# Performance work log

Measured on AMD Instinct MI355X. Metric: run time of the kernel, lower is better.

Reference implementation:

```python
import jax, jax.numpy as jnp
import numpy as np


def setup_inputs() -> dict:
    key = jax.random.key(0)
    ks = jax.random.split(key, 8)
    B, E, R, D, H = 8, 50000, 1000, 128, 256
    return {
        "head": jax.random.randint(ks[0], (B,), 0, E),
        "relation": jax.random.randint(ks[1], (B,), 0, R),
        "k": 10,
        "ent_emb": jax.random.normal(ks[2], (E, D), jnp.float32),
        "rel_emb": jax.random.normal(ks[3], (R, D), jnp.float32),
        "W1": jax.random.normal(ks[4], (3 * D, H), jnp.float32) * 0.05,
        "b1": jax.random.normal(ks[5], (H,), jnp.float32) * 0.05,
        "W2": jax.random.normal(ks[6], (H,), jnp.float32) * 0.05,
        "b2": jax.random.normal(ks[7], (1,), jnp.float32) * 0.05,
    }


def reference(head, relation, k, ent_emb, rel_emb, W1, b1, W2, b2):
    D = ent_emb.shape[1]
    # score_net first layer on cat([h, r, t]) == h@W1h + r@W1r + t@W1t (same math,
    # avoids materializing the [B*E, 3D] concat).
    W1h, W1r, W1t = W1[:D], W1[D:2 * D], W1[2 * D:]
    h = ent_emb[head]            # [B, D]
    r = rel_emb[relation]        # [B, D]
    ph = h @ W1h + r @ W1r + b1  # [B, H] -- head/relation part, computed once
    pt = ent_emb @ W1t           # [E, H] -- tail part over all entities
    hidden = jax.nn.relu(ph[:, None, :] + pt[None, :, :])   # [B, E, H]
    scores = jnp.einsum('beh,h->be', hidden, W2) + b2[0]     # [B, E]
    top_scores, top_indices = jax.lax.top_k(scores, k)
    return top_indices, top_scores
```

## Files before the change

### kernel.cpp

```cpp
#include <hip/hip_runtime.h>

#define D 128
#define HDIM 256
#define NB 8
#define NSHARD 32
#define CPS 16
#define NCAND (NSHARD * CPS)
#define PHW 16
#define WPAD 136

typedef short bf16x8 __attribute__((ext_vector_type(8)));
typedef float f32x4 __attribute__((ext_vector_type(4)));

__device__ __forceinline__ unsigned short f2bf(float x) {
    unsigned u = __float_as_uint(x);
    unsigned r = u + 0x7FFF + ((u >> 16) & 1);
    return (unsigned short)(r >> 16);
}
__device__ __forceinline__ bf16x8 pack_bf8(float4 u, float4 v) {
    union { bf16x8 v8; unsigned short s[8]; } r;
    r.s[0] = f2bf(u.x); r.s[1] = f2bf(u.y); r.s[2] = f2bf(u.z); r.s[3] = f2bf(u.w);
    r.s[4] = f2bf(v.x); r.s[5] = f2bf(v.y); r.s[6] = f2bf(v.z); r.s[7] = f2bf(v.w);
    return r.v8;
}

__device__ __forceinline__ unsigned long long sk_encode(float v, int idx) {
    unsigned u = __float_as_uint(v);
    u = (u & 0x80000000u) ? ~u : (u | 0x80000000u);
    return ((unsigned long long)u << 32) | (unsigned)(0xFFFFFFFFu - (unsigned)idx);
}
__device__ __forceinline__ float sk_val(unsigned long long key) {
    const unsigned u = (unsigned)(key >> 32);
    return (u & 0x80000000u) ? __uint_as_float(u & 0x7FFFFFFFu) : __uint_as_float(~u);
}
__device__ __forceinline__ int sk_idx(unsigned long long key) {
    return (int)(0xFFFFFFFFu - (unsigned)(key & 0xFFFFFFFFu));
}
__device__ __forceinline__ unsigned long long wave_max64(unsigned long long m) {
#pragma unroll
    for (int s = 32; s > 0; s >>= 1) {
        const unsigned long long o = __shfl_xor(m, s, 64);
        if (o > m) m = o;
    }
    return m;
}

__global__ __launch_bounds__(HDIM) void prep_kernel(
        const int* __restrict__ head, const int* __restrict__ relation,
        const float* __restrict__ ent_emb, const float* __restrict__ rel_emb,
        const float* __restrict__ W1, const float* __restrict__ b1,
        const float* __restrict__ W2, float* __restrict__ phW,
        unsigned short* __restrict__ w1tt) {
    const int w = blockIdx.x;
    const int tid = threadIdx.x;
    if (w < NB) {
        const int b = w;
        const long hidx = head[b];
        const long ridx = relation[b];
        const float* hrow = ent_emb + hidx * D;
        const float* rrow = rel_emb + ridx * D;
        float acc = b1[tid];
#pragma unroll 8
        for (int d = 0; d < D; ++d)
            acc += hrow[d] * W1[d * HDIM + tid];
#pragma unroll 8
        for (int d = 0; d < D; ++d)
            acc += rrow[d] * W1[(D + d) * HDIM + tid];
        phW[tid * PHW + b] = acc;
        if (b == 0) phW[tid * PHW + 8] = W2[tid];
    } else {
        const int k0 = (w - NB) * 4;
        const float* w1t = W1 + 2 * D * HDIM;
        unsigned short pk[4];
#pragma unroll
        for (int j = 0; j < 4; ++j)
            pk[j] = f2bf(w1t[(k0 + j) * HDIM + tid]);
        *(ushort4*)(w1tt + tid * D + k0) = make_ushort4(pk[0], pk[1], pk[2], pk[3]);
    }
}

__global__ __launch_bounds__(512, 2) void score_kernel(
        const float* __restrict__ ent_emb, const unsigned short* __restrict__ w1tt,
        const float* __restrict__ phW, float* __restrict__ scores, int E) {
    __shared__ __align__(16) unsigned short wL[HDIM][WPAD];
    __shared__ float phB[NB][HDIM];
    __shared__ float w2L[HDIM];

    const int tid = threadIdx.x;
    const int lane = tid & 63;
    const int wave = tid >> 6;
    const int lm = lane & 15;
    const int q = lane >> 4;
    const int base_e = blockIdx.x * 128 + wave * 16;

    const float* arow = ent_emb + (size_t)min(base_e + lm, E - 1) * D;
    bf16x8 aF[4];
#pragma unroll
    for (int kk = 0; kk < 4; ++kk) {
        const float4 u = *(const float4*)(arow + kk * 32 + q * 8);
        const float4 v = *(const float4*)(arow + kk * 32 + q * 8 + 4);
        aF[kk] = pack_bf8(u, v);
    }

#pragma unroll
    for (int i = 0; i < 8; ++i) {
        const int c = i * 512 + tid;
        const int row = c >> 4;
        const int col = (c & 15) << 3;
        *(uint4*)(&wL[row][col]) = *(const uint4*)(w1tt + row * D + col);
    }
    if (tid < HDIM) {
        const float4 p0 = *(const float4*)(phW + tid * PHW);
        const float4 p1 = *(const float4*)(phW + tid * PHW + 4);
        phB[0][tid] = p0.x; phB[1][tid] = p0.y; phB[2][tid] = p0.z; phB[3][tid] = p0.w;
        phB[4][tid] = p1.x; phB[5][tid] = p1.y; phB[6][tid] = p1.z; phB[7][tid] = p1.w;
        w2L[tid] = phW[tid * PHW + 8];
    }
    __syncthreads();

    float sp[NB * 4];
#pragma unroll
    for (int i = 0; i < NB * 4; ++i) sp[i] = 0.f;

#pragma unroll
    for (int t = 0; t < 16; ++t) {
        const int h = t * 16 + lm;
        bf16x8 bF[4];
#pragma unroll
        for (int kk = 0; kk < 4; ++kk)
            bF[kk] = *(const bf16x8*)(&wL[h][kk * 32 + q * 8]);

        float phv[8];
#pragma unroll
        for (int b = 0; b < NB; ++b) phv[b] = phB[b][h];
        const float w2v = w2L[h];

        f32x4 acc = (f32x4){0.f, 0.f, 0.f, 0.f};
#pragma unroll
        for (int kk = 0; kk < 4; ++kk)
            acc = __builtin_amdgcn_mfma_f32_16x16x32_bf16(aF[kk], bF[kk], acc, 0, 0, 0);

#pragma unroll
        for (int b = 0; b < NB; ++b)
#pragma unroll
            for (int r = 0; r < 4; ++r)
                sp[b * 4 + r] += fmaxf(phv[b] + acc[r], 0.f) * w2v;
    }

#pragma unroll
    for (int m = 1; m <= 8; m <<= 1) {
#pragma unroll
        for (int i = 0; i < NB * 4; ++i)
            sp[i] += __shfl_xor(sp[i], m, 64);
    }
    if (lm == 0) {
#pragma unroll
        for (int r = 0; r < 4; ++r) {
            const int e = base_e + q * 4 + r;
            if (e < E) {
#pragma unroll
                for (int b = 0; b < NB; ++b)
                    scores[(size_t)b * E + e] = sp[b * 4 + r];
            }
        }
    }
}

__global__ __launch_bounds__(256) void topk_rescore_kernel(
        const float* __restrict__ scores, int E,
        const float* __restrict__ ent_emb, const float* __restrict__ W1,
        const float* __restrict__ phW, const float* __restrict__ b2,
        unsigned long long* __restrict__ cand_exact) {
    const int b = blockIdx.x >> 5;
    const int s = blockIdx.x & 31;
    const int tid = threadIdx.x;
    const int lane = tid & 63;
    const int wave = tid >> 6;

    __shared__ unsigned long long cl[4 * CPS];
    __shared__ unsigned long long candk[CPS];
    __shared__ int eIdxs[CPS];
    __shared__ float entR[CPS][D];
    __shared__ float red[4][CPS];

    {
        const int shard = (E + NSHARD - 1) / NSHARD;
        const int start = s * shard;
        const int end = min(E, start + shard);
        const float* row = scores + (size_t)b * E;

        unsigned long long keys[CPS];
#pragma unroll
        for (int i = 0; i < CPS; ++i) keys[i] = 0ull;

        for (int e = start + tid; e < end; e += 256) {
            unsigned long long key = sk_encode(row[e], e);
            if (key > keys[CPS - 1]) {
#pragma unroll
                for (int j = 0; j < CPS; ++j) {
                    const bool gt = key > keys[j];
                    const unsigned long long mx = gt ? key : keys[j];
                    key = gt ? keys[j] : key;
                    keys[j] = mx;
                }
            }
        }
        for (int r = 0; r < CPS; ++r) {
            const unsigned long long m = wave_max64(keys[0]);
            if (keys[0] == m) {
#pragma unroll
                for (int j = 0; j < CPS - 1; ++j) keys[j] = keys[j + 1];
                keys[CPS - 1] = 0ull;
            }
            if (lane == 0) cl[wave * CPS + r] = m;
        }
        __syncthreads();
        if (wave == 0) {
            unsigned long long v = cl[lane];
            for (int r = 0; r < CPS; ++r) {
                const unsigned long long m = wave_max64(v);
                if (v == m) v = 0ull;
                if (lane == 0) candk[r] = m;
            }
        }
        __syncthreads();
    }

    if (tid < CPS) eIdxs[tid] = sk_idx(candk[tid]);
    __syncthreads();
    for (int t = tid; t < CPS * (D / 4); t += 256) {
        const int row = t >> 5, c4 = (t & 31) * 4;
        *(float4*)(&entR[row][c4]) =
            *(const float4*)(ent_emb + (size_t)eIdxs[row] * D + c4);
    }
    __syncthreads();

    const float* w1t = W1 + 2 * D * HDIM;
    float acc[CPS];
#pragma unroll
    for (int c = 0; c < CPS; ++c) acc[c] = 0.f;
    for (int d0 = 0; d0 < D; d0 += 4) {
        float w[4];
#pragma unroll
        for (int j = 0; j < 4; ++j) w[j] = w1t[(d0 + j) * HDIM + tid];
#pragma unroll
        for (int c = 0; c < CPS; ++c) {
            const float4 f = *(const float4*)(&entR[c][d0]);
            acc[c] += f.x * w[0] + f.y * w[1] + f.z * w[2] + f.w * w[3];
        }
    }
    const float phv = phW[tid * PHW + b];
    const float w2v = phW[tid * PHW + 8];
    float sc[CPS];
#pragma unroll
    for (int c = 0; c < CPS; ++c) sc[c] = fmaxf(acc[c] + phv, 0.f) * w2v;

#pragma unroll
    for (int m = 1; m <= 32; m <<= 1)
#pragma unroll
        for (int c = 0; c < CPS; ++c) sc[c] += __shfl_xor(sc[c], m, 64);
    if (lane == 0)
#pragma unroll
        for (int c = 0; c < CPS; ++c) red[wave][c] = sc[c];
    __syncthreads();
    if (tid < CPS) {
        const float v = red[0][tid] + red[1][tid] + red[2][tid] + red[3][tid] + b2[0];
        cand_exact[(size_t)(b * NSHARD + s) * CPS + tid] = sk_encode(v, eIdxs[tid]);
    }
}

__global__ __launch_bounds__(256) void final_kernel(
        const unsigned long long* __restrict__ cand_exact, int k,
        float* __restrict__ out) {
    const int lane = threadIdx.x & 63;
    const int wave = threadIdx.x >> 6;
    for (int b = wave; b < NB; b += 4) {
        unsigned long long lk[8];
#pragma unroll
        for (int j = 0; j < 8; ++j)
            lk[j] = cand_exact[(size_t)b * NCAND + j * 64 + lane];
#pragma unroll
        for (int i = 0; i < 8; ++i)
#pragma unroll
            for (int j = 0; j < 7; ++j)
                if (lk[j] < lk[j + 1]) {
                    const unsigned long long t = lk[j];
                    lk[j] = lk[j + 1];
                    lk[j + 1] = t;
                }
        for (int r = 0; r < k; ++r) {
            const unsigned long long m = wave_max64(lk[0]);
            if (lk[0] == m) {
#pragma unroll
                for (int j = 0; j < 7; ++j) lk[j] = lk[j + 1];
                lk[7] = 0ull;
            }
            if (lane == 0) {
                out[b * k + r] = (float)sk_idx(m);
                out[NB * k + b * k + r] = sk_val(m);
            }
        }
    }
}

extern "C" void kernel_launch(void* const* d_in, const int* in_sizes, int n_in,
                              void* d_out, int out_size, void* d_ws, size_t ws_size,
                              hipStream_t stream) {
    const int*   head     = (const int*)d_in[0];
    const int*   relation = (const int*)d_in[1];
    const float* ent_emb  = (const float*)d_in[3];
    const float* rel_emb  = (const float*)d_in[4];
    const float* W1       = (const float*)d_in[5];
    const float* b1       = (const float*)d_in[6];
    const float* W2       = (const float*)d_in[7];
    const float* b2       = (const float*)d_in[8];

    const int B = in_sizes[0];
    const int E = in_sizes[3] / D;
    int k = out_size / (2 * B);
    if (k > CPS) k = CPS;

    char* ws = (char*)d_ws;
    unsigned long long* cand_exact = (unsigned long long*)ws;
    float*          phW       = (float*)(ws + 32768);
    unsigned short* w1tt      = (unsigned short*)(ws + 49152);
    float*          scores    = (float*)(ws + 114688);
    float*          out       = (float*)d_out;

    prep_kernel<<<NB + 32, HDIM, 0, stream>>>(head, relation, ent_emb, rel_emb,
                                              W1, b1, W2, phW, w1tt);
    const int nblk = (E + 127) / 128;
    score_kernel<<<nblk, 512, 0, stream>>>(ent_emb, w1tt, phW, scores, E);
    topk_rescore_kernel<<<NB * NSHARD, 256, 0, stream>>>(
        scores, E, ent_emb, W1, phW, b2, cand_exact);
    final_kernel<<<1, 256, 0, stream>>>(cand_exact, k, out);
}
```

Baseline: 155.9 us.

## Double top-k shards, shrink per-thread candidate lists, parallelize prep and final selection

Splits each score row into 64 shards instead of 32, with per-thread candidate lists shrunk to 4 entries, and replaces the serial 16-round wave reduction with a 64-lane bitonic sort. The prep kernel uses 1024-thread blocks that split the head/relation projection across four slices and reduce in shared memory. The final merge runs one block per batch row instead of one block for all rows. This aims to raise parallelism in the small tail kernels, at the cost of rescoring twice as many candidates and relying on each thread seeing at most four elements per shard.

```diff
diff --git a/kernel.cpp b/kernel.cpp
--- a/kernel.cpp
+++ b/kernel.cpp
@@ -3,8 +3,9 @@
 #define D 128
 #define HDIM 256
 #define NB 8
-#define NSHARD 32
+#define NSHARD 64
 #define CPS 16
+#define LCPS 4
 #define NCAND (NSHARD * CPS)
 #define PHW 16
 #define WPAD 136
@@ -45,37 +46,45 @@
     return m;
 }
 
-__global__ __launch_bounds__(HDIM) void prep_kernel(
+__global__ __launch_bounds__(1024) void prep_kernel(
         const int* __restrict__ head, const int* __restrict__ relation,
         const float* __restrict__ ent_emb, const float* __restrict__ rel_emb,
         const float* __restrict__ W1, const float* __restrict__ b1,
         const float* __restrict__ W2, float* __restrict__ phW,
         unsigned short* __restrict__ w1tt) {
+    __shared__ float part[4][HDIM];
     const int w = blockIdx.x;
     const int tid = threadIdx.x;
+    const int h = tid & 255;
+    const int sl = tid >> 8;
     if (w < NB) {
         const int b = w;
         const long hidx = head[b];
         const long ridx = relation[b];
         const float* hrow = ent_emb + hidx * D;
         const float* rrow = rel_emb + ridx * D;
-        float acc = b1[tid];
+        float acc = 0.f;
+        const int d0 = sl * 32;
 #pragma unroll 8
-        for (int d = 0; d < D; ++d)
-            acc += hrow[d] * W1[d * HDIM + tid];
-#pragma unroll 8
-        for (int d = 0; d < D; ++d)
-            acc += rrow[d] * W1[(D + d) * HDIM + tid];
-        phW[tid * PHW + b] = acc;
-        if (b == 0) phW[tid * PHW + 8] = W2[tid];
+        for (int dd = 0; dd < 32; ++dd) {
+            const int d = d0 + dd;
+            acc += hrow[d] * W1[d * HDIM + h];
+            acc += rrow[d] * W1[(D + d) * HDIM + h];
+        }
+        part[sl][h] = acc;
+        __syncthreads();
+        if (sl == 0) {
+            phW[h * PHW + b] = part[0][h] + part[1][h] + part[2][h] + part[3][h] + b1[h];
+            if (b == 0) phW[h * PHW + 8] = W2[h];
+        }
     } else {
-        const int k0 = (w - NB) * 4;
+        const int k0 = (w - NB) * 16 + sl * 4;
         const float* w1t = W1 + 2 * D * HDIM;
         unsigned short pk[4];
 #pragma unroll
         for (int j = 0; j < 4; ++j)
-            pk[j] = f2bf(w1t[(k0 + j) * HDIM + tid]);
-        *(ushort4*)(w1tt + tid * D + k0) = make_ushort4(pk[0], pk[1], pk[2], pk[3]);
+            pk[j] = f2bf(w1t[(k0 + j) * HDIM + h]);
+        *(ushort4*)(w1tt + h * D + k0) = make_ushort4(pk[0], pk[1], pk[2], pk[3]);
     }
 }
 
@@ -171,8 +180,8 @@
         const float* __restrict__ ent_emb, const float* __restrict__ W1,
         const float* __restrict__ phW, const float* __restrict__ b2,
         unsigned long long* __restrict__ cand_exact) {
-    const int b = blockIdx.x >> 5;
-    const int s = blockIdx.x & 31;
+    const int b = blockIdx.x >> 6;
+    const int s = blockIdx.x & 63;
     const int tid = threadIdx.x;
     const int lane = tid & 63;
     const int wave = tid >> 6;
@@ -189,15 +198,15 @@
         const int end = min(E, start + shard);
         const float* row = scores + (size_t)b * E;
 
-        unsigned long long keys[CPS];
-#pragma unroll
-        for (int i = 0; i < CPS; ++i) keys[i] = 0ull;
+        unsigned long long keys[LCPS];
+#pragma unroll
+        for (int i = 0; i < LCPS; ++i) keys[i] = 0ull;
 
         for (int e = start + tid; e < end; e += 256) {
             unsigned long long key = sk_encode(row[e], e);
-            if (key > keys[CPS - 1]) {
-#pragma unroll
-                for (int j = 0; j < CPS; ++j) {
+            if (key > keys[LCPS - 1]) {
+#pragma unroll
+                for (int j = 0; j < LCPS; ++j) {
                     const bool gt = key > keys[j];
                     const unsigned long long mx = gt ? key : keys[j];
                     key = gt ? keys[j] : key;
@@ -209,19 +218,26 @@
             const unsigned long long m = wave_max64(keys[0]);
             if (keys[0] == m) {
 #pragma unroll
-                for (int j = 0; j < CPS - 1; ++j) keys[j] = keys[j + 1];
-                keys[CPS - 1] = 0ull;
+                for (int j = 0; j < LCPS - 1; ++j) keys[j] = keys[j + 1];
+                keys[LCPS - 1] = 0ull;
             }
             if (lane == 0) cl[wave * CPS + r] = m;
         }
         __syncthreads();
         if (wave == 0) {
             unsigned long long v = cl[lane];
-            for (int r = 0; r < CPS; ++r) {
-                const unsigned long long m = wave_max64(v);
-                if (v == m) v = 0ull;
-                if (lane == 0) candk[r] = m;
-            }
+#pragma unroll
+            for (int kk = 2; kk <= 64; kk <<= 1) {
+#pragma unroll
+                for (int j = kk >> 1; j > 0; j >>= 1) {
+                    const unsigned long long o = __shfl_xor(v, j, 64);
+                    const bool keep_min = (((lane & j) == 0) == ((lane & kk) != 0));
+                    const unsigned long long mn = v < o ? v : o;
+                    const unsigned long long mx = v < o ? o : v;
+                    v = keep_min ? mn : mx;
+                }
+            }
+            if (lane < CPS) candk[lane] = v;
         }
         __syncthreads();
     }
@@ -269,36 +285,34 @@
     }
 }
 
-__global__ __launch_bounds__(256) void final_kernel(
+__global__ __launch_bounds__(64) void final_kernel(
         const unsigned long long* __restrict__ cand_exact, int k,
         float* __restrict__ out) {
-    const int lane = threadIdx.x & 63;
-    const int wave = threadIdx.x >> 6;
-    for (int b = wave; b < NB; b += 4) {
-        unsigned long long lk[8];
-#pragma unroll
-        for (int j = 0; j < 8; ++j)
-            lk[j] = cand_exact[(size_t)b * NCAND + j * 64 + lane];
-#pragma unroll
-        for (int i = 0; i < 8; ++i)
-#pragma unroll
-            for (int j = 0; j < 7; ++j)
-                if (lk[j] < lk[j + 1]) {
-                    const unsigned long long t = lk[j];
-                    lk[j] = lk[j + 1];
-                    lk[j + 1] = t;
-                }
-        for (int r = 0; r < k; ++r) {
-            const unsigned long long m = wave_max64(lk[0]);
-            if (lk[0] == m) {
-#pragma unroll
-                for (int j = 0; j < 7; ++j) lk[j] = lk[j + 1];
-                lk[7] = 0ull;
-            }
-            if (lane == 0) {
-                out[b * k + r] = (float)sk_idx(m);
-                out[NB * k + b * k + r] = sk_val(m);
-            }
+    const int lane = threadIdx.x;
+    const int b = blockIdx.x;
+    unsigned long long lk[CPS];
+#pragma unroll
+    for (int j = 0; j < CPS; ++j)
+        lk[j] = cand_exact[(size_t)b * NCAND + j * 64 + lane];
+#pragma unroll
+    for (int i = 0; i < CPS - 1; ++i)
+#pragma unroll
+        for (int j = i + 1; j < CPS; ++j)
+            if (lk[i] < lk[j]) {
+                const unsigned long long t = lk[i];
+                lk[i] = lk[j];
+                lk[j] = t;
+            }
+    for (int r = 0; r < k; ++r) {
+        const unsigned long long m = wave_max64(lk[0]);
+        if (lk[0] == m) {
+#pragma unroll
+            for (int j = 0; j < CPS - 1; ++j) lk[j] = lk[j + 1];
+            lk[CPS - 1] = 0ull;
+        }
+        if (lane == 0) {
+            out[b * k + r] = (float)sk_idx(m);
+            out[NB * k + b * k + r] = sk_val(m);
         }
     }
 }
@@ -322,16 +336,16 @@
 
     char* ws = (char*)d_ws;
     unsigned long long* cand_exact = (unsigned long long*)ws;
-    float*          phW       = (float*)(ws + 32768);
-    unsigned short* w1tt      = (unsigned short*)(ws + 49152);
-    float*          scores    = (float*)(ws + 114688);
+    float*          phW       = (float*)(ws + 65536);
+    unsigned short* w1tt      = (unsigned short*)(ws + 81920);
+    float*          scores    = (float*)(ws + 147456);
     float*          out       = (float*)d_out;
 
-    prep_kernel<<<NB + 32, HDIM, 0, stream>>>(head, relation, ent_emb, rel_emb,
-                                              W1, b1, W2, phW, w1tt);
+    prep_kernel<<<NB + 8, 1024, 0, stream>>>(head, relation, ent_emb, rel_emb,
+                                             W1, b1, W2, phW, w1tt);
     const int nblk = (E + 127) / 128;
     score_kernel<<<nblk, 512, 0, stream>>>(ent_emb, w1tt, phW, scores, E);
     topk_rescore_kernel<<<NB * NSHARD, 256, 0, stream>>>(
         scores, E, ent_emb, W1, phW, b2, cand_exact);
-    final_kernel<<<1, 256, 0, stream>>>(cand_exact, k, out);
-}
+    final_kernel<<<NB, 64, 0, stream>>>(cand_exact, k, out);
+}
```

Result: faster. 139.3 us (-10.6%).
